# Performance work log

Hardware: AMD Instinct MI355X
Metric: run time of the kernel (lower is better)

Reference implementation:

```python
import jax, jax.numpy as jnp
import numpy as np

DIM, K, G, PAD = 384, 3, 4, 1
KK = K * K
EPS = 1e-5


def _deform_conv(x, offset, weight):
    # x: [B,C,H,W]; offset: [B,G*2*KK,H,W] (per group: (dy,dx) per tap); weight: [Cout,Cin,K,K]
    B, C, H, W = x.shape
    Cg = C // G
    off = offset.reshape(B, G, KK, 2, H, W)
    dy, dx = off[:, :, :, 0], off[:, :, :, 1]            # [B,G,KK,H,W]
    ky = (jnp.arange(KK) // K - PAD).astype(x.dtype).reshape(1, 1, KK, 1, 1)
    kx = (jnp.arange(KK) % K - PAD).astype(x.dtype).reshape(1, 1, KK, 1, 1)
    py = dy + ky + jnp.arange(H, dtype=x.dtype).reshape(1, 1, 1, H, 1)
    px = dx + kx + jnp.arange(W, dtype=x.dtype).reshape(1, 1, 1, 1, W)

    y0 = jnp.floor(py); x0 = jnp.floor(px)
    iy0 = y0.astype(jnp.int32); ix0 = x0.astype(jnp.int32)
    wy1 = py - y0; wx1 = px - x0
    img = x.reshape(B, G, Cg, H * W)[:, :, :, None, :]   # [B,G,Cg,1,HW]

    def corner(iy, ix, w):
        valid = (iy >= 0) & (iy < H) & (ix >= 0) & (ix < W)
        idx = (jnp.clip(iy, 0, H - 1) * W + jnp.clip(ix, 0, W - 1)).reshape(B, G, 1, KK, H * W)
        vals = jnp.take_along_axis(img, idx, axis=-1)    # [B,G,Cg,KK,HW]
        wm = (w * valid.astype(x.dtype)).reshape(B, G, 1, KK, H * W)
        return vals * wm

    sampled = (corner(iy0, ix0, (1 - wy1) * (1 - wx1))
               + corner(iy0, ix0 + 1, (1 - wy1) * wx1)
               + corner(iy0 + 1, ix0, wy1 * (1 - wx1))
               + corner(iy0 + 1, ix0 + 1, wy1 * wx1))    # [B,G,Cg,KK,HW]
    sampled = sampled.reshape(B, C, KK, H * W)
    out = jnp.einsum('bckp,ock->bop', sampled, weight.reshape(C, C, KK))
    return out.reshape(B, C, H, W)


def setup_inputs() -> dict:
    key = jax.random.key(0)
    ks = jax.random.split(key, 8)
    B, H, W = 8, 32, 32
    off_ch = G * 2 * KK
    return {
        'x': jax.random.normal(ks[0], (B, H * W, DIM), jnp.float32),
        'w_off': jax.random.normal(ks[1], (off_ch, DIM, 3, 3), jnp.float32) * 0.01,
        'b_off': jnp.zeros((off_ch,), jnp.float32),
        'w_dcn': jax.random.normal(ks[2], (DIM, DIM, K, K), jnp.float32) * 0.02,
        'bn_gamma': jnp.ones((DIM,), jnp.float32) + 0.1 * jax.random.normal(ks[3], (DIM,), jnp.float32),
        'bn_beta': 0.1 * jax.random.normal(ks[4], (DIM,), jnp.float32),
        'bn_mean': 0.1 * jax.random.normal(ks[5], (DIM,), jnp.float32),
        'bn_var': jax.random.uniform(ks[6], (DIM,), jnp.float32, 0.5, 1.5),
        'w2': jax.random.normal(ks[7], (DIM, DIM), jnp.float32) * 0.05,
        'b2': jnp.zeros((DIM,), jnp.float32),
        'H': H, 'W': W,
    }


def reference(x, w_off, b_off, w_dcn, bn_gamma, bn_beta, bn_mean, bn_var, w2, b2, H, W):
    B, P, C = x.shape
    xi = x.transpose(0, 2, 1).reshape(B, C, H, W)                       # [B,C,H,W]
    offset = jax.lax.conv_general_dilated(xi, w_off, (1, 1), ((1, 1), (1, 1)),
                                          dimension_numbers=('NCHW', 'OIHW', 'NCHW'))
    offset = offset + b_off[None, :, None, None]
    y = _deform_conv(xi, offset, w_dcn)
    # eval-mode BatchNorm2d + SiLU
    scale = bn_gamma / jnp.sqrt(bn_var + EPS)
    y = y * scale[None, :, None, None] + (bn_beta - bn_mean * scale)[None, :, None, None]
    y = y * jax.nn.sigmoid(y)
    # 1x1 conv
    y = jnp.einsum('bchw,oc->bohw', y, w2) + b2[None, :, None, None]
    return y.reshape(B, C, H * W).transpose(0, 2, 1)
```

## Files before the change

kernel.cpp:

```cpp
#include <hip/hip_runtime.h>
#include <math.h>

typedef _Float16 f16;
typedef _Float16 f16x2 __attribute__((ext_vector_type(2)));
typedef _Float16 f16x4 __attribute__((ext_vector_type(4)));
typedef _Float16 f16x8 __attribute__((ext_vector_type(8)));
typedef float f32x4 __attribute__((ext_vector_type(4)));

#define EPS_ 1e-5f

#define N_XP   3551232
#define N_WDCN 1327104
#define N_WOFF 331776
#define N_W2   147456
#define N_OFFS 589824
#define N_YH   3145728
#define N_AS   28311552

#define WS_NEED ((size_t)(N_XP + N_WDCN + N_WOFF + N_W2 + N_AS + N_YH) * 2 + (size_t)N_OFFS * 4)

static __device__ __forceinline__ f16x8 sp8(f16 h) { return (f16x8){h,h,h,h,h,h,h,h}; }

#define GLD_LDS16(g, l) __builtin_amdgcn_global_load_lds( \
    (const __attribute__((address_space(1))) void*)(g),   \
    (__attribute__((address_space(3))) void*)(l), 16, 0, 0)

#define VMCNT(N) asm volatile("s_waitcnt vmcnt(" #N ")" ::: "memory")

#define PK_X   786432
#define PK_XP  101376
#define PK_WD  147456
#define PK_WO  27648
#define PK_WZ  10368
#define PK_W2  147456
__global__ void k_pack(const float* __restrict__ x, const float* __restrict__ w_off,
                       const float* __restrict__ w_dcn, const float* __restrict__ w2,
                       f16* __restrict__ xp, f16* __restrict__ woffp,
                       f16* __restrict__ wdcnp, f16* __restrict__ w2p) {
    long i = (long)blockIdx.x * 256 + threadIdx.x;
    if (i < PK_X) {
        float4 v = ((const float4*)x)[i];
        f16x4 hv; hv.x = (f16)v.x; hv.y = (f16)v.y; hv.z = (f16)v.z; hv.w = (f16)v.w;
        int m = (int)(i / 96), c4 = (int)(i % 96);
        int b = m >> 10, h = (m >> 5) & 31, w = m & 31;
        long idx = ((long)(b * 34 + h + 1) * 34 + (w + 1)) * 96 + c4;
        ((f16x4*)xp)[idx] = hv;
    } else if (i < PK_X + PK_XP) {
        int j = (int)(i - PK_X);
        int cell = j / 96, c4 = j % 96;
        int b = cell / 132, p = cell % 132;
        int r, cp;
        if (p < 34)       { r = 0;          cp = p; }
        else if (p < 68)  { r = 33;         cp = p - 34; }
        else if (p < 100) { r = p - 68 + 1; cp = 0; }
        else              { r = p - 100 + 1; cp = 33; }
        long idx = ((long)(b * 34 + r) * 34 + cp) * 96 + c4;
        ((f16x4*)xp)[idx] = (f16x4){};
    } else if (i < PK_X + PK_XP + PK_WD) {
        int j = (int)(i - PK_X - PK_XP);
        int c = j % 384, oc = j / 384;
#pragma unroll
        for (int kk = 0; kk < 9; ++kk) {
            f16 v = (f16)w_dcn[(long)j * 9 + kk];
            wdcnp[(long)(kk * 6 + (c >> 6)) * 24576 + oc * 64 + (c & 63)] = v;
        }
    } else if (i < PK_X + PK_XP + PK_WD + PK_WO) {
        int j = (int)(i - PK_X - PK_XP - PK_WD);
        int c = j % 384, oc = j / 384;
#pragma unroll
        for (int kk = 0; kk < 9; ++kk) {
            f16 v = (f16)w_off[(long)j * 9 + kk];
            woffp[(long)(kk * 6 + (c >> 6)) * 6144 + oc * 64 + (c & 63)] = v;
        }
    } else if (i < PK_X + PK_XP + PK_WD + PK_WO + PK_WZ) {
        int j = (int)(i - PK_X - PK_XP - PK_WD - PK_WO);
        int ck = j / 192, r = j % 192;
        *(f16x8*)(&woffp[(long)ck * 6144 + 72 * 64 + r * 8]) = (f16x8){};
    } else if (i < PK_X + PK_XP + PK_WD + PK_WO + PK_WZ + PK_W2) {
        long j = i - (PK_X + PK_XP + PK_WD + PK_WO + PK_WZ);
        int kc = (int)(j & 63); long r = j >> 6;
        int oc = (int)(r % 384); int cc = (int)(r / 384);
        w2p[j] = (f16)w2[(long)oc * 384 + cc * 64 + kc];
    }
}

__global__ __launch_bounds__(256, 2) void k_off_gemm4(
        const f16* __restrict__ xp, const f16* __restrict__ wp,
        float* __restrict__ part) {
    __shared__ __attribute__((aligned(16))) f16 As[4][64 * 64];
    __shared__ __attribute__((aligned(16))) f16 Bs[4][96 * 64];
    int t = threadIdx.x;
    int bx = blockIdx.x;
    int ks = blockIdx.y;
    bx = (bx & 7) * 16 + (bx >> 3);
    int m0 = bx * 64;
    int w = t >> 6, l = t & 63, lr = l & 15, lq = l >> 4;
    int wmi = w & 1, wni = w >> 1;
    f32x4 acc[2][3] = {};

    const f16* a_base[2];
#pragma unroll
    for (int i = 0; i < 2; ++i) {
        int f = i * 256 + t;
        int ml = f >> 3, c8 = f & 7;
        int m = m0 + ml;
        int b = m >> 10, h = (m >> 5) & 31, ww = m & 31;
        a_base[i] = xp + ((long)(b * 34 + h + 1) * 34 + (ww + 1)) * 384 + ((c8 ^ (ml & 7)) * 8);
    }
    const f16* b_src[3];
#pragma unroll
    for (int i = 0; i < 3; ++i) {
        int f = i * 256 + t;
        int oc = f >> 3, c8 = f & 7;
        b_src[i] = wp + (long)oc * 64 + ((c8 ^ (oc & 7)) * 8);
    }

    int s_ck = (54 * ks) >> 2, e_ck = (54 * (ks + 1)) >> 2;
    int nck = e_ck - s_ck;

    auto stage = [&](int j, int buf) {
        int ck = s_ck + j;
        int kk = ck / 6, cc = ck % 6;
        int kkd = ((kk / 3 - 1) * 34 + (kk % 3 - 1)) * 384 + cc * 64;
#pragma unroll
        for (int i = 0; i < 2; ++i)
            GLD_LDS16(a_base[i] + kkd, &As[buf][i * 2048 + w * 512]);
#pragma unroll
        for (int i = 0; i < 3; ++i)
            GLD_LDS16(b_src[i] + (long)ck * 6144, &Bs[buf][i * 2048 + w * 512]);
    };
    auto compute = [&](int buf) {
        const char* Ab = (const char*)&As[buf][0];
        const char* Bb = (const char*)&Bs[buf][0];
        __builtin_amdgcn_s_setprio(1);
#pragma unroll
        for (int s = 0; s < 2; ++s) {
            int j = (s << 2) | lq;
            int swz = (j ^ (lr & 7)) * 16;
            f16x8 af[2], bf[3];
#pragma unroll
            for (int mi = 0; mi < 2; ++mi)
                af[mi] = *(const f16x8*)(Ab + (wmi * 32 + mi * 16 + lr) * 128 + swz);
#pragma unroll
            for (int n = 0; n < 3; ++n)
                bf[n] = *(const f16x8*)(Bb + (wni * 48 + n * 16 + lr) * 128 + swz);
#pragma unroll
            for (int mi = 0; mi < 2; ++mi)
#pragma unroll
                for (int n = 0; n < 3; ++n)
                    acc[mi][n] = __builtin_amdgcn_mfma_f32_16x16x32_f16(af[mi], bf[n], acc[mi][n], 0, 0, 0);
        }
        __builtin_amdgcn_s_setprio(0);
    };

    stage(0, 0);
    stage(1, 1);
    for (int j = 0; j < nck; ++j) {
        if (j + 2 < nck) {
            stage(j + 2, (j + 2) & 3);
            VMCNT(10);
        } else if (j + 1 < nck) {
            VMCNT(5);
        } else {
            VMCNT(0);
        }
        __builtin_amdgcn_s_barrier();
        compute(j & 3);
    }
    float* pb = part + (long)ks * (96 * 8192);
#pragma unroll
    for (int n = 0; n < 3; ++n) {
        int oc = wni * 48 + 16 * n + lr;
#pragma unroll
        for (int mi = 0; mi < 2; ++mi) {
            int m = m0 + wmi * 32 + 16 * mi + 4 * lq;
            *(f32x4*)(&pb[(long)oc * 8192 + m]) = acc[mi][n];
        }
    }
}

__global__ __launch_bounds__(256) void k_off_reduce(
        const float* __restrict__ part, const float* __restrict__ b_off,
        float* __restrict__ offs) {
    int j = blockIdx.x * 256 + threadIdx.x;
    int oc = j >> 11;
    int mq = (j & 2047) << 2;
    const long S = 96L * 8192;
    f32x4 s0 = *(const f32x4*)(&part[(long)oc * 8192 + mq]);
    f32x4 s1 = *(const f32x4*)(&part[S + (long)oc * 8192 + mq]);
    f32x4 s2 = *(const f32x4*)(&part[2 * S + (long)oc * 8192 + mq]);
    f32x4 s3 = *(const f32x4*)(&part[3 * S + (long)oc * 8192 + mq]);
    f32x4 s = s0 + s1 + s2 + s3;
    float b = b_off[oc];
#pragma unroll
    for (int r = 0; r < 4; ++r)
        offs[(long)(mq + r) * 72 + oc] = s[r] + b;
}

__global__ __launch_bounds__(256) void k_sample(
        const f16* __restrict__ xp, const float* __restrict__ offs,
        f16* __restrict__ A_t) {
    int t = threadIdx.x;
    int bid = blockIdx.x;
    int kk0 = (bid >> 8) * 3;
    int mgRaw = bid & 255;
    int mg = (mgRaw & 7) * 32 + (mgRaw >> 3);
    int mbase = mg * 32;
#pragma unroll
    for (int it = 0; it < 3; ++it) {
        int tau = it * 256 + t;
        int sh = tau & 1;
        int g = (tau >> 1) & 3;
        int q = tau >> 3;
        int kkl = q % 3;
        int m_l = q / 3;
        int m = mbase + m_l;
        int kk = kk0 + kkl;
        int b = m >> 10, h = (m >> 5) & 31, wp = m & 31;
        int tile = m >> 6, row = m & 63;
        const float2 o = *(const float2*)(offs + (long)m * 72 + (g * 9 + kk) * 2);
        float py = o.x + (float)(h + kk / 3 - 1);
        float px = o.y + (float)(wp + kk % 3 - 1);
        float fy = floorf(py), fx = floorf(px);
        int iy0 = (int)fy, ix0 = (int)fx;
        float wy1 = py - fy, wx1 = px - fx;
        float wy0 = 1.f - wy1, wx0 = 1.f - wx1;
        bool vy0 = iy0 >= 0 && iy0 < 32, vy1 = iy0 + 1 >= 0 && iy0 + 1 < 32;
        bool vx0 = ix0 >= 0 && ix0 < 32, vx1 = ix0 + 1 >= 0 && ix0 + 1 < 32;
        int cy0 = min(max(iy0, 0), 31), cy1 = min(max(iy0 + 1, 0), 31);
        int cx0 = min(max(ix0, 0), 31), cx1 = min(max(ix0 + 1, 0), 31);
        int c0 = g * 96 + sh * 48;
        const f16* s0 = xp + ((long)(b * 34 + cy0 + 1) * 34 + cx0 + 1) * 384 + c0;
        const f16* s1 = xp + ((long)(b * 34 + cy0 + 1) * 34 + cx1 + 1) * 384 + c0;
        const f16* s2 = xp + ((long)(b * 34 + cy1 + 1) * 34 + cx0 + 1) * 384 + c0;
        const f16* s3 = xp + ((long)(b * 34 + cy1 + 1) * 34 + cx1 + 1) * 384 + c0;
        f16x8 W00 = sp8((f16)(wy0 * wx0 * ((vy0 && vx0) ? 1.f : 0.f)));
        f16x8 W01 = sp8((f16)(wy0 * wx1 * ((vy0 && vx1) ? 1.f : 0.f)));
        f16x8 W10 = sp8((f16)(wy1 * wx0 * ((vy1 && vx0) ? 1.f : 0.f)));
        f16x8 W11 = sp8((f16)(wy1 * wx1 * ((vy1 && vx1) ? 1.f : 0.f)));
        long tkbase = ((long)tile * 54 + kk * 6) * 4096 + row * 64;
#pragma unroll
        for (int sg = 0; sg < 6; ++sg) {
            int c = c0 + 8 * sg;
            int cc = c >> 6, c64 = c & 63, c8 = c64 >> 3;
            f16x8 v0 = *(const f16x8*)(s0 + 8 * sg);
            f16x8 v1 = *(const f16x8*)(s1 + 8 * sg);
            f16x8 v2 = *(const f16x8*)(s2 + 8 * sg);
            f16x8 v3 = *(const f16x8*)(s3 + 8 * sg);
            f16x8 ov = v0 * W00 + v1 * W01 + v2 * W10 + v3 * W11;
            *(f16x8*)(A_t + tkbase + (long)cc * 4096 + ((c8 ^ (row & 7)) * 8)) = ov;
        }
    }
}

__global__ __launch_bounds__(256, 2) void k_dcn_gemm2(
        const f16* __restrict__ A_t, const f16* __restrict__ Bp,
        const float* __restrict__ bng, const float* __restrict__ bnb,
        const float* __restrict__ bnm, const float* __restrict__ bnv,
        f16* __restrict__ yh) {
    __shared__ __attribute__((aligned(16))) f16 As[4][64 * 64];
    __shared__ __attribute__((aligned(16))) f16 Bs[4][96 * 64];
    int t = threadIdx.x;
    int bx = blockIdx.x;
    bx = (bx & 7) * 16 + (bx >> 3);
    int m0 = bx * 64;
    int n0 = blockIdx.y * 96;
    int w = t >> 6, l = t & 63, lr = l & 15, lq = l >> 4;
    int wmi = w & 1, wni = w >> 1;
    f32x4 acc[2][3] = {};

    const f16* a_base = A_t + (long)bx * 54 * 4096 + t * 8;
    const f16* b_src[3];
#pragma unroll
    for (int i = 0; i < 3; ++i) {
        int f = i * 256 + t;
        int oc = f >> 3, c8 = f & 7;
        b_src[i] = Bp + (long)(n0 + oc) * 64 + ((c8 ^ (oc & 7)) * 8);
    }

    auto stage = [&](int ck, int buf) {
#pragma unroll
        for (int i = 0; i < 2; ++i)
            GLD_LDS16(a_base + (long)ck * 4096 + i * 2048, &As[buf][i * 2048 + w * 512]);
#pragma unroll
        for (int i = 0; i < 3; ++i)
            GLD_LDS16(b_src[i] + (long)ck * 24576, &Bs[buf][i * 2048 + w * 512]);
    };
    auto compute = [&](int buf) {
        const char* Ab = (const char*)&As[buf][0];
        const char* Bb = (const char*)&Bs[buf][0];
        __builtin_amdgcn_s_setprio(1);
#pragma unroll
        for (int s = 0; s < 2; ++s) {
            int j = (s << 2) | lq;
            int swz = (j ^ (lr & 7)) * 16;
            f16x8 af[2], bf[3];
#pragma unroll
            for (int mi = 0; mi < 2; ++mi)
                af[mi] = *(const f16x8*)(Ab + (wmi * 32 + mi * 16 + lr) * 128 + swz);
#pragma unroll
            for (int n = 0; n < 3; ++n)
                bf[n] = *(const f16x8*)(Bb + (wni * 48 + n * 16 + lr) * 128 + swz);
#pragma unroll
            for (int mi = 0; mi < 2; ++mi)
#pragma unroll
                for (int n = 0; n < 3; ++n)
                    acc[mi][n] = __builtin_amdgcn_mfma_f32_16x16x32_f16(af[mi], bf[n], acc[mi][n], 0, 0, 0);
        }
        __builtin_amdgcn_s_setprio(0);
    };

    stage(0, 0);
    stage(1, 1);
    for (int ck = 0; ck < 54; ++ck) {
        if (ck + 2 < 54) {
            stage(ck + 2, (ck + 2) & 3);
            VMCNT(10);
        } else if (ck + 1 < 54) {
            VMCNT(5);
        } else {
            VMCNT(0);
        }
        __builtin_amdgcn_s_barrier();
        compute(ck & 3);
    }
#pragma unroll
    for (int n = 0; n < 3; ++n) {
        int oc = n0 + wni * 48 + n * 16 + lr;
        float sc = bng[oc] * rsqrtf(bnv[oc] + EPS_);
        float shf = bnb[oc] - bnm[oc] * sc;
#pragma unroll
        for (int mi = 0; mi < 2; ++mi)
#pragma unroll
            for (int r = 0; r < 4; ++r) {
                int m = m0 + wmi * 32 + mi * 16 + 4 * lq + r;
                float v = acc[mi][n][r] * sc + shf;
                v = v / (1.f + __expf(-v));
                yh[(long)m * 384 + oc] = (f16)v;
            }
    }
}

__global__ __launch_bounds__(512, 2) void k_dcn_fused(
        const f16* __restrict__ xp, const float* __restrict__ offs,
        const f16* __restrict__ wp,
        const float* __restrict__ bng, const float* __restrict__ bnb,
        const float* __restrict__ bnm, const float* __restrict__ bnv,
        f16* __restrict__ yh) {
    __shared__ __attribute__((aligned(16))) f16 As[2][64 * 72];
    __shared__ __attribute__((aligned(16))) int ca[2][4][64][4];
    __shared__ __attribute__((aligned(16))) f16x4 cwl[2][4][64];
    int t = threadIdx.x;
    int bx = blockIdx.x;
    bx = (bx & 7) * 16 + (bx >> 3);
    int m0 = bx * 64;
    int n0 = blockIdx.y * 192;
    int w = t >> 6, l = t & 63, lr = l & 15, lq = l >> 4;
    int wm = (w & 1) * 32, wn = (w >> 1) * 48;
    int spx = t >> 3, slot = t & 7;
    const char* xb = (const char*)xp;
    f32x4 acc[2][3] = {};

    auto coords = [&](int kkn, int bufn) {
        if (t < 256) {
            int g = t >> 6, px = t & 63;
            int m = m0 + px;
            int b = m >> 10, h = (m >> 5) & 31, wwp = m & 31;
            int ky = kkn / 3 - 1, kx = kkn % 3 - 1;
            const float2 o = *(const float2*)(offs + (long)m * 72 + (g * 9 + kkn) * 2);
            float py = o.x + (float)(h + ky);
            float pxx = o.y + (float)(wwp + kx);
            float fy = floorf(py), fx = floorf(pxx);
            int iy0 = (int)fy, ix0 = (int)fx;
            float wy1 = py - fy, wx1 = pxx - fx;
            float wy0 = 1.f - wy1, wx0 = 1.f - wx1;
            bool vy0 = iy0 >= 0 && iy0 < 32, vy1 = iy0 + 1 >= 0 && iy0 + 1 < 32;
            bool vx0 = ix0 >= 0 && ix0 < 32, vx1 = ix0 + 1 >= 0 && ix0 + 1 < 32;
            int cy0 = min(max(iy0, 0), 31), cy1 = min(max(iy0 + 1, 0), 31);
            int cx0 = min(max(ix0, 0), 31), cx1 = min(max(ix0 + 1, 0), 31);
            ca[bufn][g][px][0] = ((b * 34 + cy0 + 1) * 34 + cx0 + 1) * 768;
            ca[bufn][g][px][1] = ((b * 34 + cy0 + 1) * 34 + cx1 + 1) * 768;
            ca[bufn][g][px][2] = ((b * 34 + cy1 + 1) * 34 + cx0 + 1) * 768;
            ca[bufn][g][px][3] = ((b * 34 + cy1 + 1) * 34 + cx1 + 1) * 768;
            f16x4 wv;
            wv.x = (f16)(wy0 * wx0 * ((vy0 && vx0) ? 1.f : 0.f));
            wv.y = (f16)(wy0 * wx1 * ((vy0 && vx1) ? 1.f : 0.f));
            wv.z = (f16)(wy1 * wx0 * ((vy1 && vx0) ? 1.f : 0.f));
            wv.w = (f16)(wy1 * wx1 * ((vy1 && vx1) ? 1.f : 0.f));
            cwl[bufn][g][px] = wv;
        }
    };

    coords(0, 0);
    __syncthreads();
    {
        int cst = 8 * slot;
        int g = cst / 96;
        int4 cv = *(const int4*)(&ca[0][g][spx][0]);
        f16x4 wv = cwl[0][g][spx];
        long cb = (long)(cst * 2);
        f16x8 v0 = *(const f16x8*)(xb + cv.x + cb);
        f16x8 v1 = *(const f16x8*)(xb + cv.y + cb);
        f16x8 v2 = *(const f16x8*)(xb + cv.z + cb);
        f16x8 v3 = *(const f16x8*)(xb + cv.w + cb);
        f16x8 sv = v0 * sp8(wv.x) + v1 * sp8(wv.y) + v2 * sp8(wv.z) + v3 * sp8(wv.w);
        *(f16x8*)(&As[0][spx * 72 + 8 * slot]) = sv;
    }
    int cur = 0, kk = 0, cc = 0;
    for (int ck = 0; ck < 54; ++ck) {
        __syncthreads();
        bool hn = ck < 53;
        int kk2 = kk + (cc == 5), cc2 = (cc == 5) ? 0 : (cc + 1);
        f16x8 v0, v1, v2, v3; f16x4 wv;
        if (hn) {
            int cst = cc2 * 64 + 8 * slot;
            int g = cst / 96;
            int kb = kk2 & 1;
            int4 cv = *(const int4*)(&ca[kb][g][spx][0]);
            wv = cwl[kb][g][spx];
            long cb = (long)(cst * 2);
            v0 = *(const f16x8*)(xb + cv.x + cb);
            v1 = *(const f16x8*)(xb + cv.y + cb);
            v2 = *(const f16x8*)(xb + cv.z + cb);
            v3 = *(const f16x8*)(xb + cv.w + cb);
        }
        if (cc == 4 && kk < 8) coords(kk + 1, (kk + 1) & 1);
        const f16* wbase = wp + (long)ck * (384 * 64);
#pragma unroll
        for (int s = 0; s < 2; ++s) {
            f16x8 a0 = *(const f16x8*)(&As[cur][(wm + lr) * 72 + 32 * s + 8 * lq]);
            f16x8 a1 = *(const f16x8*)(&As[cur][(wm + 16 + lr) * 72 + 32 * s + 8 * lq]);
#pragma unroll
            for (int n = 0; n < 3; ++n) {
                f16x8 b = *(const f16x8*)(wbase + (long)(n0 + wn + 16 * n + lr) * 64 + 32 * s + 8 * lq);
                acc[0][n] = __builtin_amdgcn_mfma_f32_16x16x32_f16(a0, b, acc[0][n], 0, 0, 0);
                acc[1][n] = __builtin_amdgcn_mfma_f32_16x16x32_f16(a1, b, acc[1][n], 0, 0, 0);
            }
        }
        if (hn) {
            f16x8 sv = v0 * sp8(wv.x) + v1 * sp8(wv.y) + v2 * sp8(wv.z) + v3 * sp8(wv.w);
            *(f16x8*)(&As[cur ^ 1][spx * 72 + 8 * slot]) = sv;
        }
        cur ^= 1; kk = kk2; cc = cc2;
    }
#pragma unroll
    for (int n = 0; n < 3; ++n) {
        int oc = n0 + wn + 16 * n + lr;
        float sc = bng[oc] * rsqrtf(bnv[oc] + EPS_);
        float sh = bnb[oc] - bnm[oc] * sc;
#pragma unroll
        for (int mi = 0; mi < 2; ++mi)
#pragma unroll
            for (int r = 0; r < 4; ++r) {
                int m = m0 + wm + 16 * mi + 4 * lq + r;
                float v = acc[mi][n][r] * sc + sh;
                v = v / (1.f + __expf(-v));
                yh[(long)m * 384 + oc] = (f16)v;
            }
    }
}

__global__ __launch_bounds__(256, 2) void k_out_gemm3(
        const f16* __restrict__ yh, const f16* __restrict__ wp,
        const float* __restrict__ b2, float* __restrict__ out) {
    __shared__ __attribute__((aligned(16))) f16 As[4][64 * 64];
    __shared__ __attribute__((aligned(16))) f16 Bs[4][96 * 64];
    int t = threadIdx.x;
    int bx = blockIdx.x;
    bx = (bx & 7) * 16 + (bx >> 3);
    int m0 = bx * 64;
    int n0 = blockIdx.y * 96;
    int w = t >> 6, l = t & 63, lr = l & 15, lq = l >> 4;
    int wmi = w & 1, wni = w >> 1;
    f32x4 acc[2][3] = {};

    const f16* a_src[2];
#pragma unroll
    for (int i = 0; i < 2; ++i) {
        int f = i * 256 + t;
        int ml = f >> 3, c8 = f & 7;
        a_src[i] = yh + (long)(m0 + ml) * 384 + ((c8 ^ (ml & 7)) * 8);
    }
    const f16* b_src[3];
#pragma unroll
    for (int i = 0; i < 3; ++i) {
        int f = i * 256 + t;
        int oc = f >> 3, c8 = f & 7;
        b_src[i] = wp + (long)(n0 + oc) * 64 + ((c8 ^ (oc & 7)) * 8);
    }

    auto stage = [&](int cc, int buf) {
#pragma unroll
        for (int i = 0; i < 2; ++i)
            GLD_LDS16(a_src[i] + cc * 64, &As[buf][i * 2048 + w * 512]);
#pragma unroll
        for (int i = 0; i < 3; ++i)
            GLD_LDS16(b_src[i] + (long)cc * 24576, &Bs[buf][i * 2048 + w * 512]);
    };
    auto compute = [&](int buf) {
        const char* Ab = (const char*)&As[buf][0];
        const char* Bb = (const char*)&Bs[buf][0];
        __builtin_amdgcn_s_setprio(1);
#pragma unroll
        for (int s = 0; s < 2; ++s) {
            int j = (s << 2) | lq;
            int swz = (j ^ (lr & 7)) * 16;
            f16x8 af[2], bf[3];
#pragma unroll
            for (int mi = 0; mi < 2; ++mi)
                af[mi] = *(const f16x8*)(Ab + (wmi * 32 + mi * 16 + lr) * 128 + swz);
#pragma unroll
            for (int n = 0; n < 3; ++n)
                bf[n] = *(const f16x8*)(Bb + (wni * 48 + n * 16 + lr) * 128 + swz);
#pragma unroll
            for (int mi = 0; mi < 2; ++mi)
#pragma unroll
                for (int n = 0; n < 3; ++n)
                    acc[mi][n] = __builtin_amdgcn_mfma_f32_16x16x32_f16(af[mi], bf[n], acc[mi][n], 0, 0, 0);
        }
        __builtin_amdgcn_s_setprio(0);
    };

    stage(0, 0);
    stage(1, 1);
    for (int cc = 0; cc < 6; ++cc) {
        if (cc + 2 < 6) {
            stage(cc + 2, (cc + 2) & 3);
            VMCNT(10);
        } else if (cc + 1 < 6) {
            VMCNT(5);
        } else {
            VMCNT(0);
        }
        __builtin_amdgcn_s_barrier();
        compute(cc & 3);
    }
#pragma unroll
    for (int n = 0; n < 3; ++n) {
        int oc = n0 + wni * 48 + 16 * n + lr;
        float bia = b2[oc];
#pragma unroll
        for (int mi = 0; mi < 2; ++mi)
#pragma unroll
            for (int r = 0; r < 4; ++r) {
                int m = m0 + wmi * 32 + 16 * mi + 4 * lq + r;
                out[(long)m * 384 + oc] = acc[mi][n][r] + bia;
            }
    }
}

extern "C" void kernel_launch(void* const* d_in, const int* in_sizes, int n_in,
                              void* d_out, int out_size, void* d_ws, size_t ws_size,
                              hipStream_t stream) {
    const float* x        = (const float*)d_in[0];
    const float* w_off    = (const float*)d_in[1];
    const float* b_off    = (const float*)d_in[2];
    const float* w_dcn    = (const float*)d_in[3];
    const float* bn_gamma = (const float*)d_in[4];
    const float* bn_beta  = (const float*)d_in[5];
    const float* bn_mean  = (const float*)d_in[6];
    const float* bn_var   = (const float*)d_in[7];
    const float* w2       = (const float*)d_in[8];
    const float* b2       = (const float*)d_in[9];

    char* ws = (char*)d_ws;
    f16*   xp    = (f16*)ws;                                  ws += (size_t)N_XP * 2;
    f16*   wdcnp = (f16*)ws;                                  ws += (size_t)N_WDCN * 2;
    f16*   woffp = (f16*)ws;                                  ws += (size_t)N_WOFF * 2;
    f16*   w2p   = (f16*)ws;                                  ws += (size_t)N_W2 * 2;
    float* offs  = (float*)ws;                                ws += (size_t)N_OFFS * 4;
    f16*   yh    = (f16*)ws;                                  ws += (size_t)N_YH * 2;
    f16*   A_t   = (f16*)ws;
    bool big = ws_size >= WS_NEED;
    float* part = (float*)(big ? (void*)A_t : (void*)ws);

    k_pack<<<4770, 256, 0, stream>>>(x, w_off, w_dcn, w2, xp, woffp, wdcnp, w2p);
    k_off_gemm4<<<dim3(128, 4), 256, 0, stream>>>(xp, woffp, part);
    k_off_reduce<<<576, 256, 0, stream>>>(part, b_off, offs);

    if (big) {
        k_sample<<<768, 256, 0, stream>>>(xp, offs, A_t);
        k_dcn_gemm2<<<dim3(128, 4), 256, 0, stream>>>(A_t, wdcnp,
                bn_gamma, bn_beta, bn_mean, bn_var, yh);
    } else {
        k_dcn_fused<<<dim3(128, 2), 512, 0, stream>>>(xp, offs, wdcnp,
                bn_gamma, bn_beta, bn_mean, bn_var, yh);
    }
    k_out_gemm3<<<dim3(128, 4), 256, 0, stream>>>(yh, w2p, b2, (float*)d_out);
}
```

Measured before the change: 99.79 us.

## Restructure deformable sampling kernel with shared-memory corner tables and coalesced stores

Splits the sampling kernel into two phases. First, each thread computes bilinear corner addresses and weights for one (row, group) pair and stores them in shared memory. Then threads cooperatively gather 8-channel chunks so that each group of 8 lanes writes a full contiguous 128-byte row of the swizzled A_t tile, which should coalesce stores better than the old per-thread 48-channel strided pattern. The grid changes to 128x9 blocks (64 rows per block, one tap each), and the cost is an added __syncthreads plus shared-memory reads.

```diff
diff --git a/kernel.cpp b/kernel.cpp
--- a/kernel.cpp
+++ b/kernel.cpp
@@ -200,27 +200,20 @@
 __global__ __launch_bounds__(256) void k_sample(
         const f16* __restrict__ xp, const float* __restrict__ offs,
         f16* __restrict__ A_t) {
+    __shared__ int   cad[64][4][4];
+    __shared__ f16x4 cwd[64][4];
     int t = threadIdx.x;
-    int bid = blockIdx.x;
-    int kk0 = (bid >> 8) * 3;
-    int mgRaw = bid & 255;
-    int mg = (mgRaw & 7) * 32 + (mgRaw >> 3);
-    int mbase = mg * 32;
-#pragma unroll
-    for (int it = 0; it < 3; ++it) {
-        int tau = it * 256 + t;
-        int sh = tau & 1;
-        int g = (tau >> 1) & 3;
-        int q = tau >> 3;
-        int kkl = q % 3;
-        int m_l = q / 3;
-        int m = mbase + m_l;
-        int kk = kk0 + kkl;
-        int b = m >> 10, h = (m >> 5) & 31, wp = m & 31;
-        int tile = m >> 6, row = m & 63;
+    int raw = blockIdx.x;
+    int bx = (raw & 7) * 16 + (raw >> 3);
+    int kk = blockIdx.y;
+    int m0 = bx * 64;
+    {
+        int row = t & 63, g = t >> 6;
+        int m = m0 + row;
+        int b = m >> 10, h = (m >> 5) & 31, wpix = m & 31;
         const float2 o = *(const float2*)(offs + (long)m * 72 + (g * 9 + kk) * 2);
         float py = o.x + (float)(h + kk / 3 - 1);
-        float px = o.y + (float)(wp + kk % 3 - 1);
+        float px = o.y + (float)(wpix + kk % 3 - 1);
         float fy = floorf(py), fx = floorf(px);
         int iy0 = (int)fy, ix0 = (int)fx;
         float wy1 = py - fy, wx1 = px - fx;
@@ -229,26 +222,37 @@
         bool vx0 = ix0 >= 0 && ix0 < 32, vx1 = ix0 + 1 >= 0 && ix0 + 1 < 32;
         int cy0 = min(max(iy0, 0), 31), cy1 = min(max(iy0 + 1, 0), 31);
         int cx0 = min(max(ix0, 0), 31), cx1 = min(max(ix0 + 1, 0), 31);
-        int c0 = g * 96 + sh * 48;
-        const f16* s0 = xp + ((long)(b * 34 + cy0 + 1) * 34 + cx0 + 1) * 384 + c0;
-        const f16* s1 = xp + ((long)(b * 34 + cy0 + 1) * 34 + cx1 + 1) * 384 + c0;
-        const f16* s2 = xp + ((long)(b * 34 + cy1 + 1) * 34 + cx0 + 1) * 384 + c0;
-        const f16* s3 = xp + ((long)(b * 34 + cy1 + 1) * 34 + cx1 + 1) * 384 + c0;
-        f16x8 W00 = sp8((f16)(wy0 * wx0 * ((vy0 && vx0) ? 1.f : 0.f)));
-        f16x8 W01 = sp8((f16)(wy0 * wx1 * ((vy0 && vx1) ? 1.f : 0.f)));
-        f16x8 W10 = sp8((f16)(wy1 * wx0 * ((vy1 && vx0) ? 1.f : 0.f)));
-        f16x8 W11 = sp8((f16)(wy1 * wx1 * ((vy1 && vx1) ? 1.f : 0.f)));
-        long tkbase = ((long)tile * 54 + kk * 6) * 4096 + row * 64;
-#pragma unroll
-        for (int sg = 0; sg < 6; ++sg) {
-            int c = c0 + 8 * sg;
-            int cc = c >> 6, c64 = c & 63, c8 = c64 >> 3;
-            f16x8 v0 = *(const f16x8*)(s0 + 8 * sg);
-            f16x8 v1 = *(const f16x8*)(s1 + 8 * sg);
-            f16x8 v2 = *(const f16x8*)(s2 + 8 * sg);
-            f16x8 v3 = *(const f16x8*)(s3 + 8 * sg);
-            f16x8 ov = v0 * W00 + v1 * W01 + v2 * W10 + v3 * W11;
-            *(f16x8*)(A_t + tkbase + (long)cc * 4096 + ((c8 ^ (row & 7)) * 8)) = ov;
+        cad[row][g][0] = ((b * 34 + cy0 + 1) * 34 + cx0 + 1) * 768;
+        cad[row][g][1] = ((b * 34 + cy0 + 1) * 34 + cx1 + 1) * 768;
+        cad[row][g][2] = ((b * 34 + cy1 + 1) * 34 + cx0 + 1) * 768;
+        cad[row][g][3] = ((b * 34 + cy1 + 1) * 34 + cx1 + 1) * 768;
+        f16x4 wv;
+        wv.x = (f16)(wy0 * wx0 * ((vy0 && vx0) ? 1.f : 0.f));
+        wv.y = (f16)(wy0 * wx1 * ((vy0 && vx1) ? 1.f : 0.f));
+        wv.z = (f16)(wy1 * wx0 * ((vy1 && vx0) ? 1.f : 0.f));
+        wv.w = (f16)(wy1 * wx1 * ((vy1 && vx1) ? 1.f : 0.f));
+        cwd[row][g] = wv;
+    }
+    __syncthreads();
+    int rb = t >> 3, w8 = t & 7;
+    const char* xb = (const char*)xp;
+    long obase = ((long)bx * 54 + (long)kk * 6) * 4096;
+#pragma unroll
+    for (int cc = 0; cc < 6; ++cc) {
+        int c = cc * 64 + 8 * w8;
+        int g = c / 96;
+        long cb = (long)c * 2;
+#pragma unroll
+        for (int rr = 0; rr < 2; ++rr) {
+            int r = 2 * rb + rr;
+            const int* ca = cad[r][g];
+            f16x4 wv = cwd[r][g];
+            f16x8 v0 = *(const f16x8*)(xb + ca[0] + cb);
+            f16x8 v1 = *(const f16x8*)(xb + ca[1] + cb);
+            f16x8 v2 = *(const f16x8*)(xb + ca[2] + cb);
+            f16x8 v3 = *(const f16x8*)(xb + ca[3] + cb);
+            f16x8 ov = v0 * sp8(wv.x) + v1 * sp8(wv.y) + v2 * sp8(wv.z) + v3 * sp8(wv.w);
+            *(f16x8*)(A_t + obase + cc * 4096 + r * 64 + ((w8 ^ (r & 7)) * 8)) = ov;
         }
     }
 }
@@ -579,7 +583,7 @@
     k_off_reduce<<<576, 256, 0, stream>>>(part, b_off, offs);
 
     if (big) {
-        k_sample<<<768, 256, 0, stream>>>(xp, offs, A_t);
+        k_sample<<<dim3(128, 9), 256, 0, stream>>>(xp, offs, A_t);
         k_dcn_gemm2<<<dim3(128, 4), 256, 0, stream>>>(A_t, wdcnp,
                 bn_gamma, bn_beta, bn_mean, bn_var, yh);
     } else {
```

Result: faster. 84.09 us (median of 2 runs) (-15.7%).
